# Performance work log

Measured on AMD Instinct MI355X. Metric: run time of the kernel, lower is better.

## Reference

```python
import jax, jax.numpy as jnp
import numpy as np

N = 4_000_000
EPS = 1e-6

# Quaternion layout: (w, x, y, z)

def _qmul(q1, q2):
    w1, v1 = q1[..., :1], q1[..., 1:]
    w2, v2 = q2[..., :1], q2[..., 1:]
    w = w1 * w2 - jnp.sum(v1 * v2, axis=-1, keepdims=True)
    v = w1 * v2 + w2 * v1 + jnp.cross(v1, v2)
    return jnp.concatenate([w, v], axis=-1)

def _qinv(q):
    # unit quaternion inverse = conjugate
    return q * jnp.array([1.0, -1.0, -1.0, -1.0], dtype=q.dtype)

def _qlog(q):
    # SO(3) log map: returns tangent vector theta * axis, shape [..., 3]
    w, v = q[..., 0], q[..., 1:]
    nv = jnp.linalg.norm(v, axis=-1)
    small = nv < EPS
    nv_safe = jnp.where(small, 1.0, nv)
    theta = 2.0 * jnp.arctan2(nv, w)
    # small-angle limit: theta/nv -> 2/w
    scale = jnp.where(small, 2.0 / w, theta / nv_safe)
    return v * scale[..., None]

def setup_inputs() -> dict:
    key = jax.random.key(0)
    k1, k2 = jax.random.split(key)
    a = jax.random.normal(k1, (N, 4), dtype=jnp.float32)
    a = a / jnp.linalg.norm(a, axis=-1, keepdims=True)
    idd = jax.random.normal(k2, (N, 4), dtype=jnp.float32)
    idd = idd / jnp.linalg.norm(idd, axis=-1, keepdims=True)
    return {"a": a, "idd": idd}

def reference(a, idd):
    # (a.Inv() @ idd).Log().norm()
    rel = _qmul(_qinv(a), idd)          # [N,4] relative rotation
    tangent = _qlog(rel)                 # [N,3] log map
    return jnp.linalg.norm(tangent)      # scalar Frobenius norm
```

## Files before the change

kernel.cpp:

```cpp
#include <hip/hip_runtime.h>
#include <math.h>


__global__ __launch_bounds__(256) void geo_loss_kernel(
        const float4* __restrict__ a,
        const float4* __restrict__ idd,
        float* __restrict__ ws, int n) {
    float acc = 0.0f;
    int stride = gridDim.x * blockDim.x;
    for (int i = blockIdx.x * blockDim.x + threadIdx.x; i < n; i += stride) {
        float4 qa = a[i];
        float4 qb = idd[i];
        float w1 = qa.x, x1 = -qa.y, y1 = -qa.z, z1 = -qa.w;
        float w2 = qb.x, x2 = qb.y,  y2 = qb.z,  z2 = qb.w;
        float w  = w1*w2 - (x1*x2 + y1*y2 + z1*z2);
        float vx = w1*x2 + w2*x1 + (y1*z2 - z1*y2);
        float vy = w1*y2 + w2*y1 + (z1*x2 - x1*z2);
        float vz = w1*z2 + w2*z1 + (x1*y2 - y1*x2);
        float nv2 = vx*vx + vy*vy + vz*vz;
        float nv = sqrtf(nv2);
        float t;
        if (nv < 1e-6f) {
            float s = 2.0f / w;
            t = nv2 * s * s;
        } else {
            float theta = 2.0f * atan2f(nv, w);
            t = theta * theta;
        }
        acc += t;
    }
    #pragma unroll
    for (int off = 32; off > 0; off >>= 1)
        acc += __shfl_down(acc, off, 64);
    __shared__ float smem[4];
    int lane = threadIdx.x & 63;
    int wid  = threadIdx.x >> 6;
    if (lane == 0) smem[wid] = acc;
    __syncthreads();
    if (threadIdx.x == 0) {
        float s = smem[0] + smem[1] + smem[2] + smem[3];
        atomicAdd(ws, s);
    }
}

__global__ void finalize_kernel(const float* __restrict__ ws,
                                float* __restrict__ out) {
    out[0] = sqrtf(ws[0]);
}

extern "C" void kernel_launch(void* const* d_in, const int* in_sizes, int n_in,
                              void* d_out, int out_size, void* d_ws, size_t ws_size,
                              hipStream_t stream) {
    const float4* a   = (const float4*)d_in[0];
    const float4* idd = (const float4*)d_in[1];
    int n = in_sizes[0] / 4;
    float* ws = (float*)d_ws;

    hipMemsetAsync(ws, 0, sizeof(float), stream);

    const int block = 256;
    const int grid  = 2048;
    geo_loss_kernel<<<grid, block, 0, stream>>>(a, idd, ws, n);
    finalize_kernel<<<1, 1, 0, stream>>>(ws, (float*)d_out);
}
```

Baseline: 159.7 us.

## Unroll loads, approximate atan2 via acos polynomial, fuse finalize into last block

Swaps atan2f for a rsqrt-normalised cosine plus a short polynomial acos approximation, which is cheaper but less accurate. Batches eight independent float4 loads per thread to raise memory-level parallelism. Sizes the grid so each thread handles eight elements, and drops the separate finalize kernel by having the last block (tracked with an atomic counter) write the sqrt. The polynomial approximation adds error of roughly 1e-4 rad per element, which may matter for tolerance checks.

Result: slower. 211.0 us (+32.1%).

```diff
diff --git a/kernel.cpp b/kernel.cpp
--- a/kernel.cpp
+++ b/kernel.cpp
@@ -1,51 +1,75 @@
 #include <hip/hip_runtime.h>
 #include <math.h>
 
+#define BLOCK 256
+#define UNROLL 8
 
-__global__ __launch_bounds__(256) void geo_loss_kernel(
+__device__ __forceinline__ float theta_sq(float4 qa, float4 qb) {
+    float w1 = qa.x, x1 = -qa.y, y1 = -qa.z, z1 = -qa.w;
+    float w2 = qb.x, x2 = qb.y,  y2 = qb.z,  z2 = qb.w;
+    float w  = w1*w2 - (x1*x2 + y1*y2 + z1*z2);
+    float vx = w1*x2 + w2*x1 + (y1*z2 - z1*y2);
+    float vy = w1*y2 + w2*y1 + (z1*x2 - x1*z2);
+    float vz = w1*z2 + w2*z1 + (x1*y2 - y1*x2);
+    float nv2 = vx*vx + vy*vy + vz*vz;
+    float nv  = sqrtf(nv2);
+    if (nv < 1e-6f) {
+        float s = 2.0f / w;
+        return nv2 * s * s;
+    }
+    float rn = rsqrtf(w*w + nv2);
+    float c  = w * rn;
+    float ac = fabsf(c);
+    float p  = ((-0.0187293f*ac + 0.0742610f)*ac - 0.2121144f)*ac + 1.5707288f;
+    float r  = sqrtf(fmaxf(1.0f - ac, 0.0f)) * p;
+    float acosc = (c >= 0.0f) ? r : (3.14159265358979f - r);
+    float theta = 2.0f * acosc;
+    return theta * theta;
+}
+
+__global__ __launch_bounds__(BLOCK) void geo_loss_kernel(
         const float4* __restrict__ a,
         const float4* __restrict__ idd,
-        float* __restrict__ ws, int n) {
+        float* __restrict__ ws,
+        float* __restrict__ out,
+        int n, int nblocks) {
+    const int stride = gridDim.x * BLOCK;
+    const int i0 = blockIdx.x * BLOCK + threadIdx.x;
     float acc = 0.0f;
-    int stride = gridDim.x * blockDim.x;
-    for (int i = blockIdx.x * blockDim.x + threadIdx.x; i < n; i += stride) {
-        float4 qa = a[i];
-        float4 qb = idd[i];
-        float w1 = qa.x, x1 = -qa.y, y1 = -qa.z, z1 = -qa.w;
-        float w2 = qb.x, x2 = qb.y,  y2 = qb.z,  z2 = qb.w;
-        float w  = w1*w2 - (x1*x2 + y1*y2 + z1*z2);
-        float vx = w1*x2 + w2*x1 + (y1*z2 - z1*y2);
-        float vy = w1*y2 + w2*y1 + (z1*x2 - x1*z2);
-        float vz = w1*z2 + w2*z1 + (x1*y2 - y1*x2);
-        float nv2 = vx*vx + vy*vy + vz*vz;
-        float nv = sqrtf(nv2);
-        float t;
-        if (nv < 1e-6f) {
-            float s = 2.0f / w;
-            t = nv2 * s * s;
-        } else {
-            float theta = 2.0f * atan2f(nv, w);
-            t = theta * theta;
+
+    for (int base = i0; base < n; base += UNROLL * stride) {
+        float4 qa[UNROLL], qb[UNROLL];
+        #pragma unroll
+        for (int k = 0; k < UNROLL; k++) {
+            int idx = base + k * stride;
+            if (idx < n) { qa[k] = a[idx]; qb[k] = idd[idx]; }
         }
-        acc += t;
+        #pragma unroll
+        for (int k = 0; k < UNROLL; k++) {
+            int idx = base + k * stride;
+            if (idx < n) acc += theta_sq(qa[k], qb[k]);
+        }
     }
+
     #pragma unroll
     for (int off = 32; off > 0; off >>= 1)
         acc += __shfl_down(acc, off, 64);
-    __shared__ float smem[4];
+    __shared__ float smem[BLOCK / 64];
     int lane = threadIdx.x & 63;
     int wid  = threadIdx.x >> 6;
     if (lane == 0) smem[wid] = acc;
     __syncthreads();
+
     if (threadIdx.x == 0) {
         float s = smem[0] + smem[1] + smem[2] + smem[3];
         atomicAdd(ws, s);
+        __threadfence();
+        unsigned int old = atomicAdd((unsigned int*)(ws + 1), 1u);
+        if (old == (unsigned int)nblocks - 1u) {
+            float total = atomicAdd(ws, 0.0f);
+            out[0] = sqrtf(total);
+        }
     }
-}
-
-__global__ void finalize_kernel(const float* __restrict__ ws,
-                                float* __restrict__ out) {
-    out[0] = sqrtf(ws[0]);
 }
 
 extern "C" void kernel_launch(void* const* d_in, const int* in_sizes, int n_in,
@@ -56,10 +80,8 @@
     int n = in_sizes[0] / 4;
     float* ws = (float*)d_ws;
 
-    hipMemsetAsync(ws, 0, sizeof(float), stream);
+    hipMemsetAsync(ws, 0, 2 * sizeof(float), stream);
 
-    const int block = 256;
-    const int grid  = 2048;
-    geo_loss_kernel<<<grid, block, 0, stream>>>(a, idd, ws, n);
-    finalize_kernel<<<1, 1, 0, stream>>>(ws, (float*)d_out);
+    int grid = (n + BLOCK * UNROLL - 1) / (BLOCK * UNROLL);
+    geo_loss_kernel<<<grid, BLOCK, 0, stream>>>(a, idd, ws, (float*)d_out, n, grid);
 }
```
